# Performance work log

Measured on AMD Instinct MI355X. Metric: run time of the kernel, lower is better.

The kernel has to match this reference:

```python
import jax, jax.numpy as jnp
import numpy as np

N = 100000   # nodes
E = 1600000  # edges (before self loops)
D = 128      # input_dim
H1 = 128     # hidden_dim_1
H2 = 128     # hidden_dim_2
OUT = 1      # output_dim
G = 64       # number of graphs in the batch


def setup_inputs() -> dict:
    key = jax.random.key(0)
    ks = jax.random.split(key, 11)
    x = jax.random.normal(ks[0], (N, D), dtype=jnp.float32)
    edge_index = jax.random.randint(ks[1], (2, E), 0, N, dtype=jnp.int64)
    batch = jnp.sort(jax.random.randint(ks[2], (N,), 0, G, dtype=jnp.int64))
    s = 0.05
    W1 = jax.random.normal(ks[3], (D, H1), dtype=jnp.float32) * s
    b1 = jnp.zeros((H1,), dtype=jnp.float32)
    W2 = jax.random.normal(ks[4], (H1, H2), dtype=jnp.float32) * s
    b2 = jnp.zeros((H2,), dtype=jnp.float32)
    W_iou = jax.random.normal(ks[5], (H2, OUT), dtype=jnp.float32) * s
    b_iou = jnp.zeros((OUT,), dtype=jnp.float32)
    W_iop = jax.random.normal(ks[6], (H2, OUT), dtype=jnp.float32) * s
    b_iop = jnp.zeros((OUT,), dtype=jnp.float32)
    return dict(x=x, edge_index=edge_index, batch=batch,
                W1=W1, b1=b1, W2=W2, b2=b2,
                W_iou=W_iou, b_iou=b_iou, W_iop=W_iop, b_iop=b_iop)


def reference(x, edge_index, batch, W1, b1, W2, b2, W_iou, b_iou, W_iop, b_iop):
    n = x.shape[0]
    # add_self_loops
    loops = jnp.arange(n, dtype=edge_index.dtype)
    src = jnp.concatenate([edge_index[0], loops])
    dst = jnp.concatenate([edge_index[1], loops])
    # symmetric GCN normalization: deg over target nodes
    deg = jax.ops.segment_sum(jnp.ones_like(dst, dtype=x.dtype), dst, num_segments=n)
    dinv = jnp.where(deg > 0, jax.lax.rsqrt(deg), 0.0)
    norm = dinv[src] * dinv[dst]  # [E+N]

    def gcn_conv(h, W, b):
        hw = h @ W                                  # [N, H]
        m = hw[src] * norm[:, None]                 # gather + normalize [E+N, H]
        return jax.ops.segment_sum(m, dst, num_segments=n) + b  # scatter-add

    h = jax.nn.relu(gcn_conv(x, W1, b1))
    h = jax.nn.relu(gcn_conv(h, W2, b2))
    # global_max_pool over graph ids
    pooled = jax.ops.segment_max(h, batch, num_segments=G)
    pooled = jnp.where(jnp.isfinite(pooled), pooled, 0.0)  # guard empty graphs
    iou = pooled @ W_iou + b_iou
    iop = pooled @ W_iop + b_iop
    return jnp.concatenate([iou, iop], axis=1)  # [G, 2*OUT]
```

## Files before the change

kernel.cpp:

```cpp
#include <hip/hip_runtime.h>
#include <math.h>

typedef unsigned int u32;
typedef __attribute__((ext_vector_type(8))) short short8v;
typedef __attribute__((ext_vector_type(4))) float floatx4;

__device__ inline float blo(u32 u) { return __uint_as_float(u << 16); }
__device__ inline float bhi(u32 u) { return __uint_as_float(u & 0xffff0000u); }
__device__ inline u32 f2b(float f) {
    u32 u = __float_as_uint(f);
    return (u + 0x7fffu + ((u >> 16) & 1u)) >> 16;
}
__device__ inline u32 pack2(float a, float b) { return f2b(a) | (f2b(b) << 16); }

__global__ void init_k(u32* gcursor, int B, int CAP, u32* pooled, int np) {
    int i = blockIdx.x * blockDim.x + threadIdx.x;
    if (i < np) pooled[i] = 0u;
    if (i < B) gcursor[i] = (u32)i * (u32)CAP;
}

__global__ __launch_bounds__(256) void wprep_k(const float* __restrict__ W1, const float* __restrict__ W2,
                                               ushort* __restrict__ W1t, ushort* __restrict__ W2t) {
    int idx = blockIdx.x * 256 + threadIdx.x;
    int k = idx >> 7, j = idx & 127;
    W1t[j * 128 + k] = (ushort)f2b(W1[idx]);
    W2t[j * 128 + k] = (ushort)f2b(W2[idx]);
}

#define FILL_EPT 16
__global__ __launch_bounds__(256) void bfill_k(const int* __restrict__ src, const int* __restrict__ dst,
                                               u32* __restrict__ gcursor, u32* __restrict__ pairs,
                                               int E, int B, int CAP) {
    __shared__ u32 lcnt[256];
    __shared__ u32 lbase[256];
    const int t = threadIdx.x;
    lcnt[t] = 0;
    __syncthreads();

    const int base_e = blockIdx.x * (256 * FILL_EPT);
    u32 pk[FILL_EPT];
    u32 bk[FILL_EPT];
    u32 rk[FILL_EPT];
#pragma unroll
    for (int j = 0; j < FILL_EPT; ++j) {
        int e = base_e + t + j * 256;
        pk[j] = 0xFFFFFFFFu;
        if (e < E) {
            int d = dst[e];
            int s = src[e];
            u32 b = (u32)d >> 9;
            pk[j] = (u32)s | (((u32)d & 511u) << 17);
            bk[j] = b;
            rk[j] = atomicAdd(&lcnt[b], 1u);
        }
    }
    __syncthreads();
    if (t < B) {
        u32 v = lcnt[t];
        lbase[t] = v ? atomicAdd(&gcursor[t], v) : 0u;
    }
    __syncthreads();
#pragma unroll
    for (int j = 0; j < FILL_EPT; ++j) {
        if (pk[j] != 0xFFFFFFFFu) {
            u32 b = bk[j];
            u32 pos = lbase[b] + rk[j];
            if (pos < (b + 1u) * (u32)CAP) pairs[pos] = pk[j];
        }
    }
}

__global__ __launch_bounds__(256) void csort_k(const u32* __restrict__ pairs, const u32* __restrict__ gcursor,
                                               u32* __restrict__ csr, uint2* __restrict__ rowinfo,
                                               float* __restrict__ dinv, int N, int CAP) {
    __shared__ u32 hist[512];
    __shared__ u32 excl[512];
    __shared__ u32 pscan[256];
    const int b = blockIdx.x, t = threadIdx.x;
    const u32 base = (u32)b * (u32)CAP;
    u32 cnt = gcursor[b] - base;
    if (cnt > (u32)CAP) cnt = (u32)CAP;

    hist[t] = 0u; hist[t + 256] = 0u;
    __syncthreads();
    for (u32 j = t; j < cnt; j += 256) {
        u32 p = pairs[base + j];
        atomicAdd(&hist[p >> 17], 1u);
    }
    __syncthreads();
    u32 a = hist[2 * t], c = hist[2 * t + 1];
    u32 s = a + c;
    pscan[t] = s;
    __syncthreads();
    for (int off = 1; off < 256; off <<= 1) {
        u32 v = (t >= off) ? pscan[t - off] : 0u;
        __syncthreads();
        pscan[t] += v;
        __syncthreads();
    }
    u32 e0 = pscan[t] - s;
    excl[2 * t] = e0;
    excl[2 * t + 1] = e0 + a;
    __syncthreads();
    const int node0 = b << 9;
#pragma unroll
    for (int q = 0; q < 2; ++q) {
        int loc = t + q * 256;
        int i = node0 + loc;
        if (i < N) {
            u32 dg = hist[loc];
            rowinfo[i] = make_uint2(base + excl[loc], dg);
            dinv[i] = rsqrtf((float)(dg + 1u));
        }
    }
    __syncthreads();
    for (u32 j = t; j < cnt; j += 256) {
        u32 p = pairs[base + j];
        u32 loc = p >> 17;
        u32 pos = atomicAdd(&excl[loc], 1u);
        csr[base + pos] = p & 0x1FFFFu;
    }
}

__device__ inline int swz(int row, int kbyte) { return row * 256 + (kbyte ^ ((row & 7) << 4)); }

template <bool BF16IN>
__global__ __launch_bounds__(256) void gemm_mfma_k(const void* __restrict__ inp, const ushort* __restrict__ Wt,
                                                   ushort* __restrict__ outp, int N) {
    __shared__ char Xl[128 * 256];
    __shared__ char Wl[128 * 256];
    const int t = threadIdx.x;
    const int brow = blockIdx.x * 128;

    {
        const uint4* g = (const uint4*)Wt;
#pragma unroll
        for (int i = 0; i < 8; ++i) {
            int f = t + i * 256;
            int r = f >> 4, kb = (f & 15) << 4;
            *(uint4*)(Wl + swz(r, kb)) = g[f];
        }
    }
    if (BF16IN) {
#pragma unroll
        for (int i = 0; i < 8; ++i) {
            int f = t + i * 256;
            int r = f >> 4, kb = (f & 15) << 4;
            int gr = brow + r;
            uint4 v = make_uint4(0u, 0u, 0u, 0u);
            if (gr < N) v = ((const uint4*)inp)[gr * 16 + (kb >> 4)];
            *(uint4*)(Xl + swz(r, kb)) = v;
        }
    } else {
#pragma unroll
        for (int i = 0; i < 16; ++i) {
            int f = t + i * 256;
            int r = f >> 5, c4 = (f & 31) << 2;
            int gr = brow + r;
            uint2 v = make_uint2(0u, 0u);
            if (gr < N) {
                float4 x = ((const float4*)inp)[gr * 32 + (c4 >> 2)];
                v.x = pack2(x.x, x.y);
                v.y = pack2(x.z, x.w);
            }
            *(uint2*)(Xl + swz(r, c4 * 2)) = v;
        }
    }
    __syncthreads();

    const int lane = t & 63;
    const int wave = t >> 6;
    const int l15 = lane & 15;
    const int lk = (lane >> 4) * 16;

    floatx4 acc[2][8];
#pragma unroll
    for (int mt = 0; mt < 2; ++mt)
#pragma unroll
        for (int nt = 0; nt < 8; ++nt) acc[mt][nt] = (floatx4){0.f, 0.f, 0.f, 0.f};

#pragma unroll
    for (int ks = 0; ks < 4; ++ks) {
        int kb = ks * 64 + lk;
        short8v a[2], b[8];
#pragma unroll
        for (int mt = 0; mt < 2; ++mt) {
            int row = wave * 32 + mt * 16 + l15;
            a[mt] = *(const short8v*)(Xl + swz(row, kb));
        }
#pragma unroll
        for (int nt = 0; nt < 8; ++nt) {
            int jr = nt * 16 + l15;
            b[nt] = *(const short8v*)(Wl + swz(jr, kb));
        }
#pragma unroll
        for (int mt = 0; mt < 2; ++mt)
#pragma unroll
            for (int nt = 0; nt < 8; ++nt)
                acc[mt][nt] = __builtin_amdgcn_mfma_f32_16x16x32_bf16(a[mt], b[nt], acc[mt][nt], 0, 0, 0);
    }

    const int r0 = (lane >> 4) * 4;
#pragma unroll
    for (int mt = 0; mt < 2; ++mt) {
#pragma unroll
        for (int reg = 0; reg < 4; ++reg) {
            int grow = brow + wave * 32 + mt * 16 + r0 + reg;
            if (grow < N) {
#pragma unroll
                for (int nt = 0; nt < 8; ++nt)
                    outp[grow * 128 + nt * 16 + l15] = (ushort)f2b(acc[mt][nt][reg]);
            }
        }
    }
}

__global__ __launch_bounds__(256) void edge_accum_k(const u32* __restrict__ hw, const uint2* __restrict__ rowinfo,
                                                    const u32* __restrict__ csr, const float* __restrict__ dinv,
                                                    const float* __restrict__ bias, u32* __restrict__ hout, int N) {
    const int lane = threadIdx.x & 63;
    const int wid = (blockIdx.x * blockDim.x + threadIdx.x) >> 6;
    const int nw = (gridDim.x * blockDim.x) >> 6;
    const float2 bb = ((const float2*)bias)[lane];

    for (int i = wid; i < N; i += nw) {
        float di = dinv[i];
        u32 us = hw[i * 64 + lane];
        float di2 = di * di;
        float a0 = blo(us) * di2, a1 = bhi(us) * di2;
        uint2 ri = rowinfo[i];
        int r0 = (int)ri.x, r1 = r0 + (int)ri.y;
        for (int base = r0; base < r1; base += 64) {
            int eidx = base + lane;
            bool valid = eidx < r1;
            int sl = valid ? (int)csr[eidx] : 0;
            float wl = valid ? dinv[sl] * di : 0.f;
            int nb = min(64, r1 - base);
            int j = 0;
            for (; j + 4 <= nb; j += 4) {
                int s0 = __shfl(sl, j), s1 = __shfl(sl, j + 1), s2 = __shfl(sl, j + 2), s3 = __shfl(sl, j + 3);
                u32 u0 = hw[s0 * 64 + lane];
                u32 u1 = hw[s1 * 64 + lane];
                u32 u2 = hw[s2 * 64 + lane];
                u32 u3 = hw[s3 * 64 + lane];
                float w0 = __shfl(wl, j), w1 = __shfl(wl, j + 1), w2 = __shfl(wl, j + 2), w3 = __shfl(wl, j + 3);
                a0 = fmaf(blo(u0), w0, a0); a1 = fmaf(bhi(u0), w0, a1);
                a0 = fmaf(blo(u1), w1, a0); a1 = fmaf(bhi(u1), w1, a1);
                a0 = fmaf(blo(u2), w2, a0); a1 = fmaf(bhi(u2), w2, a1);
                a0 = fmaf(blo(u3), w3, a0); a1 = fmaf(bhi(u3), w3, a1);
            }
            for (; j < nb; ++j) {
                int s = __shfl(sl, j);
                float w = __shfl(wl, j);
                u32 u = hw[s * 64 + lane];
                a0 = fmaf(blo(u), w, a0);
                a1 = fmaf(bhi(u), w, a1);
            }
        }
        a0 = fmaxf(a0 + bb.x, 0.f);
        a1 = fmaxf(a1 + bb.y, 0.f);
        hout[i * 64 + lane] = pack2(a0, a1);
    }
}

__global__ __launch_bounds__(64) void pool_k(const u32* __restrict__ h2, const int* __restrict__ batch,
                                             u32* __restrict__ pooled, int N) {
    int lane = threadIdx.x;
    int start = blockIdx.x * 64;
    int end = min(start + 64, N);
    if (start >= N) return;
    int gcur = batch[start];
    float m0 = 0.f, m1 = 0.f;
    for (int n = start; n < end; ++n) {
        int g = batch[n];
        if (g != gcur) {
            atomicMax(pooled + gcur * 128 + lane * 2, __float_as_uint(m0));
            atomicMax(pooled + gcur * 128 + lane * 2 + 1, __float_as_uint(m1));
            gcur = g;
            m0 = m1 = 0.f;
        }
        u32 u = h2[n * 64 + lane];
        m0 = fmaxf(m0, blo(u));
        m1 = fmaxf(m1, bhi(u));
    }
    atomicMax(pooled + gcur * 128 + lane * 2, __float_as_uint(m0));
    atomicMax(pooled + gcur * 128 + lane * 2 + 1, __float_as_uint(m1));
}

__global__ void final_k(const float* __restrict__ pooled, const float* __restrict__ Wu, const float* __restrict__ bu,
                        const float* __restrict__ Wp, const float* __restrict__ bp, float* __restrict__ out) {
    int t = threadIdx.x;
    int g = t >> 1, c = t & 1;
    const float* w = c ? Wp : Wu;
    const float* pr = pooled + g * 128;
    float s = 0.f;
    for (int k = 0; k < 128; k += 4)
        s += pr[k] * w[k] + pr[k + 1] * w[k + 1] + pr[k + 2] * w[k + 2] + pr[k + 3] * w[k + 3];
    out[g * 2 + c] = s + (c ? bp[0] : bu[0]);
}

extern "C" void kernel_launch(void* const* d_in, const int* in_sizes, int n_in,
                              void* d_out, int out_size, void* d_ws, size_t ws_size,
                              hipStream_t stream) {
    const float* x     = (const float*)d_in[0];
    const int*   ei    = (const int*)d_in[1];
    const int*   batch = (const int*)d_in[2];
    const float* W1    = (const float*)d_in[3];
    const float* b1    = (const float*)d_in[4];
    const float* W2    = (const float*)d_in[5];
    const float* b2    = (const float*)d_in[6];
    const float* Wu    = (const float*)d_in[7];
    const float* bu    = (const float*)d_in[8];
    const float* Wp    = (const float*)d_in[9];
    const float* bp    = (const float*)d_in[10];
    float* out = (float*)d_out;

    const int N = in_sizes[2];
    const int E = in_sizes[1] / 2;
    const int* src = ei;
    const int* dst = ei + E;

    const int B = (N + 511) >> 9;
    int avg = E / B;
    int CAP = avg + 6 * (int)sqrt((double)avg) + 64;
    CAP = (CAP + 63) & ~63;

    char* ws = (char*)d_ws;
    size_t o = 0;
    auto alloc = [&](size_t bytes) { size_t r = o; o += (bytes + 255) & ~(size_t)255; return r; };
    u32*   gcursor = (u32*)(ws + alloc(1024));
    float* dinv    = (float*)(ws + alloc((size_t)N * 4));
    uint2* rowinfo = (uint2*)(ws + alloc((size_t)N * 8));
    u32*   csr     = (u32*)(ws + alloc((size_t)B * CAP * 4));
    ushort* hwA    = (ushort*)(ws + alloc((size_t)N * 128 * 2));
    ushort* hB     = (ushort*)(ws + alloc((size_t)N * 128 * 2));
    u32*   pooled  = (u32*)(ws + alloc(64 * 128 * 4));
    ushort* W1t    = (ushort*)(ws + alloc(128 * 128 * 2));
    ushort* W2t    = (ushort*)(ws + alloc(128 * 128 * 2));
    u32*   pairs   = (u32*)hwA;
    (void)ws_size; (void)n_in;

    const int gFill = (E + 256 * FILL_EPT - 1) / (256 * FILL_EPT);
    const int gGemm = (N + 127) / 128;
    const int gPool = (N + 63) / 64;

    init_k<<<32, 256, 0, stream>>>(gcursor, B, CAP, pooled, 64 * 128);
    wprep_k<<<64, 256, 0, stream>>>(W1, W2, W1t, W2t);
    bfill_k<<<gFill, 256, 0, stream>>>(src, dst, gcursor, pairs, E, B, CAP);
    csort_k<<<B, 256, 0, stream>>>(pairs, gcursor, csr, rowinfo, dinv, N, CAP);

    gemm_mfma_k<false><<<gGemm, 256, 0, stream>>>((const void*)x, W1t, hwA, N);
    edge_accum_k<<<2048, 256, 0, stream>>>((const u32*)hwA, rowinfo, csr, dinv, b1, (u32*)hB, N);
    gemm_mfma_k<true><<<gGemm, 256, 0, stream>>>((const void*)hB, W2t, hwA, N);
    edge_accum_k<<<2048, 256, 0, stream>>>((const u32*)hwA, rowinfo, csr, dinv, b2, (u32*)hB, N);

    pool_k<<<gPool, 64, 0, stream>>>((const u32*)hB, batch, pooled, N);
    final_k<<<1, 128, 0, stream>>>((const float*)pooled, Wu, bu, Wp, bp, out);
}
```

Measured before the change: 244.5 us.

## Fold source-side degree scaling into GEMM epilogue and simplify edge gather

The GEMM epilogue now multiplies each output row by dinv[row], so the aggregation kernel only sums neighbor rows and applies the destination dinv once at the end. This removes the per-edge dinv[src] gather and the per-edge multiply. The edge loop now reads CSR indices as wave-uniform scalars via readfirstlane instead of a lane-parallel load plus shuffles, and unrolls by 8 to keep more gathers in flight. In exchange each scaled row is rounded to bf16 before summation, which slightly changes numerics, and the scalar index loads go through the scalar path one at a time.

```diff
diff --git a/kernel.cpp b/kernel.cpp
--- a/kernel.cpp
+++ b/kernel.cpp
@@ -4,6 +4,8 @@
 typedef unsigned int u32;
 typedef __attribute__((ext_vector_type(8))) short short8v;
 typedef __attribute__((ext_vector_type(4))) float floatx4;
+
+__device__ inline int rfl(int v) { return __builtin_amdgcn_readfirstlane(v); }
 
 __device__ inline float blo(u32 u) { return __uint_as_float(u << 16); }
 __device__ inline float bhi(u32 u) { return __uint_as_float(u & 0xffff0000u); }
@@ -126,6 +128,7 @@
 
 template <bool BF16IN>
 __global__ __launch_bounds__(256) void gemm_mfma_k(const void* __restrict__ inp, const ushort* __restrict__ Wt,
+                                                   const float* __restrict__ dinv,
                                                    ushort* __restrict__ outp, int N) {
     __shared__ char Xl[128 * 256];
     __shared__ char Wl[128 * 256];
@@ -200,16 +203,17 @@
                 acc[mt][nt] = __builtin_amdgcn_mfma_f32_16x16x32_bf16(a[mt], b[nt], acc[mt][nt], 0, 0, 0);
     }
 
-    const int r0 = (lane >> 4) * 4;
+    const int r0w = (lane >> 4) * 4;
 #pragma unroll
     for (int mt = 0; mt < 2; ++mt) {
 #pragma unroll
         for (int reg = 0; reg < 4; ++reg) {
-            int grow = brow + wave * 32 + mt * 16 + r0 + reg;
+            int grow = brow + wave * 32 + mt * 16 + r0w + reg;
             if (grow < N) {
+                float sc = dinv[grow];
 #pragma unroll
                 for (int nt = 0; nt < 8; ++nt)
-                    outp[grow * 128 + nt * 16 + l15] = (ushort)f2b(acc[mt][nt][reg]);
+                    outp[grow * 128 + nt * 16 + l15] = (ushort)f2b(acc[mt][nt][reg] * sc);
             }
         }
     }
@@ -224,42 +228,49 @@
     const float2 bb = ((const float2*)bias)[lane];
 
     for (int i = wid; i < N; i += nw) {
+        uint2 ri = rowinfo[i];
+        const int r0 = rfl((int)ri.x);
+        const int deg = rfl((int)ri.y);
         float di = dinv[i];
-        u32 us = hw[i * 64 + lane];
-        float di2 = di * di;
-        float a0 = blo(us) * di2, a1 = bhi(us) * di2;
-        uint2 ri = rowinfo[i];
-        int r0 = (int)ri.x, r1 = r0 + (int)ri.y;
-        for (int base = r0; base < r1; base += 64) {
-            int eidx = base + lane;
-            bool valid = eidx < r1;
-            int sl = valid ? (int)csr[eidx] : 0;
-            float wl = valid ? dinv[sl] * di : 0.f;
-            int nb = min(64, r1 - base);
-            int j = 0;
-            for (; j + 4 <= nb; j += 4) {
-                int s0 = __shfl(sl, j), s1 = __shfl(sl, j + 1), s2 = __shfl(sl, j + 2), s3 = __shfl(sl, j + 3);
-                u32 u0 = hw[s0 * 64 + lane];
-                u32 u1 = hw[s1 * 64 + lane];
-                u32 u2 = hw[s2 * 64 + lane];
-                u32 u3 = hw[s3 * 64 + lane];
-                float w0 = __shfl(wl, j), w1 = __shfl(wl, j + 1), w2 = __shfl(wl, j + 2), w3 = __shfl(wl, j + 3);
-                a0 = fmaf(blo(u0), w0, a0); a1 = fmaf(bhi(u0), w0, a1);
-                a0 = fmaf(blo(u1), w1, a0); a1 = fmaf(bhi(u1), w1, a1);
-                a0 = fmaf(blo(u2), w2, a0); a1 = fmaf(bhi(u2), w2, a1);
-                a0 = fmaf(blo(u3), w3, a0); a1 = fmaf(bhi(u3), w3, a1);
-            }
-            for (; j < nb; ++j) {
-                int s = __shfl(sl, j);
-                float w = __shfl(wl, j);
-                u32 u = hw[s * 64 + lane];
-                a0 = fmaf(blo(u), w, a0);
-                a1 = fmaf(bhi(u), w, a1);
-            }
-        }
-        a0 = fmaxf(a0 + bb.x, 0.f);
-        a1 = fmaxf(a1 + bb.y, 0.f);
-        hout[i * 64 + lane] = pack2(a0, a1);
+        u32 us = hw[(size_t)i * 64 + lane];
+        float a0 = blo(us), a1 = bhi(us);
+
+        int j = 0;
+        for (; j + 8 <= deg; j += 8) {
+            int s0 = rfl((int)csr[r0 + j + 0]);
+            int s1 = rfl((int)csr[r0 + j + 1]);
+            int s2 = rfl((int)csr[r0 + j + 2]);
+            int s3 = rfl((int)csr[r0 + j + 3]);
+            int s4 = rfl((int)csr[r0 + j + 4]);
+            int s5 = rfl((int)csr[r0 + j + 5]);
+            int s6 = rfl((int)csr[r0 + j + 6]);
+            int s7 = rfl((int)csr[r0 + j + 7]);
+            u32 u0 = hw[(size_t)s0 * 64 + lane];
+            u32 u1 = hw[(size_t)s1 * 64 + lane];
+            u32 u2 = hw[(size_t)s2 * 64 + lane];
+            u32 u3 = hw[(size_t)s3 * 64 + lane];
+            u32 u4 = hw[(size_t)s4 * 64 + lane];
+            u32 u5 = hw[(size_t)s5 * 64 + lane];
+            u32 u6 = hw[(size_t)s6 * 64 + lane];
+            u32 u7 = hw[(size_t)s7 * 64 + lane];
+            a0 += blo(u0); a1 += bhi(u0);
+            a0 += blo(u1); a1 += bhi(u1);
+            a0 += blo(u2); a1 += bhi(u2);
+            a0 += blo(u3); a1 += bhi(u3);
+            a0 += blo(u4); a1 += bhi(u4);
+            a0 += blo(u5); a1 += bhi(u5);
+            a0 += blo(u6); a1 += bhi(u6);
+            a0 += blo(u7); a1 += bhi(u7);
+        }
+        for (; j < deg; ++j) {
+            int s = rfl((int)csr[r0 + j]);
+            u32 u = hw[(size_t)s * 64 + lane];
+            a0 += blo(u); a1 += bhi(u);
+        }
+
+        a0 = fmaxf(fmaf(a0, di, bb.x), 0.f);
+        a1 = fmaxf(fmaf(a1, di, bb.y), 0.f);
+        hout[(size_t)i * 64 + lane] = pack2(a0, a1);
     }
 }
 
@@ -349,9 +360,9 @@
     bfill_k<<<gFill, 256, 0, stream>>>(src, dst, gcursor, pairs, E, B, CAP);
     csort_k<<<B, 256, 0, stream>>>(pairs, gcursor, csr, rowinfo, dinv, N, CAP);
 
-    gemm_mfma_k<false><<<gGemm, 256, 0, stream>>>((const void*)x, W1t, hwA, N);
+    gemm_mfma_k<false><<<gGemm, 256, 0, stream>>>((const void*)x, W1t, dinv, hwA, N);
     edge_accum_k<<<2048, 256, 0, stream>>>((const u32*)hwA, rowinfo, csr, dinv, b1, (u32*)hB, N);
-    gemm_mfma_k<true><<<gGemm, 256, 0, stream>>>((const void*)hB, W2t, hwA, N);
+    gemm_mfma_k<true><<<gGemm, 256, 0, stream>>>((const void*)hB, W2t, dinv, hwA, N);
     edge_accum_k<<<2048, 256, 0, stream>>>((const u32*)hwA, rowinfo, csr, dinv, b2, (u32*)hB, N);
 
     pool_k<<<gPool, 64, 0, stream>>>((const u32*)hB, batch, pooled, N);
```

Result: no change. 246.3 us (+0.7%).
